# Kernel optimization log

Hardware: AMD Instinct MI355X
Metric: run time of the kernel (lower is better)

## Reference

```python
import jax, jax.numpy as jnp
import numpy as np

N_KERNELS = 5
MUL_FACTOR = 2.0


def setup_inputs() -> dict:
    key = jax.random.key(0)
    k1, k2 = jax.random.split(key)
    x = jax.random.normal(k1, (8192, 64), dtype=jnp.float32)
    y = jax.random.normal(k2, (8192, 64), dtype=jnp.float32)
    return {"x": x, "y": y}


def reference(x, y):
    # bandwidth multipliers: mul_factor ** (arange(n) - n//2) -> [0.25,0.5,1,2,4]
    mults = MUL_FACTOR ** (jnp.arange(N_KERNELS, dtype=jnp.float32) - N_KERNELS // 2)

    z = jnp.concatenate([x, y], axis=0)  # [N, d], N = n + m
    n = x.shape[0]
    N = z.shape[0]

    # squared pairwise L2 distances: ||a||^2 + ||b||^2 - 2 a.b, clamped at 0
    sq = jnp.sum(z * z, axis=-1)  # [N]
    d2 = jnp.maximum(sq[:, None] + sq[None, :] - 2.0 * (z @ z.T), 0.0)  # [N, N]

    # data-dependent bandwidth: sum(d2) / (N^2 - N)
    bw = jnp.sum(d2) / (N * N - N)

    # multi-bandwidth RBF kernel, summed over kernels: [N, N]
    K = jnp.sum(jnp.exp(-d2[None, :, :] / (bw * mults)[:, None, None]), axis=0)

    XX = jnp.mean(K[:n, :n])
    XY = jnp.mean(K[:n, n:])
    YY = jnp.mean(K[n:, n:])
    return XX - 2.0 * XY + YY
```

## Files before the change

kernel.cpp:

```cpp
#include <hip/hip_runtime.h>
#include <hip/hip_bf16.h>

#define D 64

typedef __attribute__((ext_vector_type(8))) _Float16 half8;
typedef __attribute__((ext_vector_type(4))) float floatx4;
typedef __attribute__((ext_vector_type(2))) float f32x2;

typedef __attribute__((address_space(1))) unsigned int gu32_t;
typedef __attribute__((address_space(3))) unsigned int lu32_t;

__global__ __launch_bounds__(256) void k_pre(const float* __restrict__ x, const float* __restrict__ y,
                                             int nx, _Float16* __restrict__ zh,
                                             float* __restrict__ sq, double* __restrict__ Tpart,
                                             float* __restrict__ Spart) {
    int tid = threadIdx.x;
    int lane = tid & 63, wid = tid >> 6;
    int t = blockIdx.x * 256 + tid;
    size_t e = (size_t)t * 8;
    int row = (int)(e >> 6);
    const float* src = (row < nx) ? (x + e) : (y + (e - (size_t)nx * D));
    float4 v0 = ((const float4*)src)[0];
    float4 v1 = ((const float4*)src)[1];
    half8 h;
    h[0]=(_Float16)v0.x; h[1]=(_Float16)v0.y; h[2]=(_Float16)v0.z; h[3]=(_Float16)v0.w;
    h[4]=(_Float16)v1.x; h[5]=(_Float16)v1.y; h[6]=(_Float16)v1.z; h[7]=(_Float16)v1.w;
    *(half8*)(zh + e) = h;
    float p = v0.x*v0.x + v0.y*v0.y + v0.z*v0.z + v0.w*v0.w
            + v1.x*v1.x + v1.y*v1.y + v1.z*v1.z + v1.w*v1.w;
    float s = p;
    s += __shfl_xor(s, 1);
    s += __shfl_xor(s, 2);
    s += __shfl_xor(s, 4);
    if ((tid & 7) == 0) sq[row] = s;

    __shared__ float colbuf[32][64];
    int rib = tid >> 3, cg = tid & 7;
    *(float4*)&colbuf[rib][cg * 8]     = v0;
    *(float4*)&colbuf[rib][cg * 8 + 4] = v1;

    double dp = (double)p;
    dp += __shfl_xor(dp, 1);
    dp += __shfl_xor(dp, 2);
    dp += __shfl_xor(dp, 4);
    dp += __shfl_xor(dp, 8);
    dp += __shfl_xor(dp, 16);
    dp += __shfl_xor(dp, 32);
    __shared__ double redw[4];
    if (lane == 0) redw[wid] = dp;
    __syncthreads();
    if (tid == 0) Tpart[blockIdx.x] = (redw[0] + redw[1]) + (redw[2] + redw[3]);

    if (tid < 64) {
        float cs = 0.f;
#pragma unroll
        for (int r2 = 0; r2 < 32; ++r2) cs += colbuf[r2][tid];
        Spart[blockIdx.x * 64 + tid] = cs;
    }
}

__global__ __launch_bounds__(256) void k_bw(const double* __restrict__ Tpart, int ntp,
                                            const float* __restrict__ Spart, int nsp,
                                            int N, float* __restrict__ cq_p) {
    int t = threadIdx.x;
    double Tp = 0.0;
    for (int b = t; b < ntp; b += 256) Tp += Tpart[b];

    int q = t >> 6, col = t & 63;
    int bpq = nsp >> 2;
    const float* sp = Spart + (size_t)(q * bpq) * 64 + col;
    float c0 = 0.f, c1 = 0.f, c2 = 0.f, c3 = 0.f;
    for (int b = 0; b < bpq; b += 4) {
        c0 += sp[(b + 0) * 64];
        c1 += sp[(b + 1) * 64];
        c2 += sp[(b + 2) * 64];
        c3 += sp[(b + 3) * 64];
    }
    __shared__ float cred[256];
    cred[t] = (c0 + c1) + (c2 + c3);

    __shared__ double red[256];
    red[t] = Tp;
    __syncthreads();
    for (int off = 128; off > 0; off >>= 1) {
        if (t < off) red[t] += red[t + off];
        __syncthreads();
    }
    double T = red[0];
    __shared__ double red2[64];
    if (t < 64) {
        float Sk = cred[t] + cred[t + 64] + cred[t + 128] + cred[t + 192];
        red2[t] = (double)Sk * (double)Sk;
    }
    __syncthreads();
    if (t == 0) {
        double S2 = 0.0;
        for (int i = 0; i < 64; ++i) S2 += red2[i];
        double sumd2 = 2.0 * (double)N * T - 2.0 * S2;
        double bw = sumd2 / ((double)N * (double)N - (double)N);
        cq_p[0] = (float)(1.4426950408889634 / (4.0 * bw));
    }
}

__global__ __launch_bounds__(256, 6) void k_mmd(const _Float16* __restrict__ zh,
                                                const float* __restrict__ sq,
                                                const float* __restrict__ cq_p,
                                                int nb, double* __restrict__ partial) {
    int bid = (nb - 1) - (int)blockIdx.x;
    int g = (int)((sqrtf(1.0f + 2.0f * (float)bid) - 1.0f) * 0.5f);
    while (2 * (g + 1) * (g + 2) <= bid) ++g;
    while (2 * g * (g + 1) > bid) --g;
    int r = bid - 2 * g * (g + 1);
    int gp1 = g + 1;
    int rig = r / gp1;
    int jc  = r - rig * gp1;
    int ib  = 4 * g + rig;

    int jstart = jc * 512;
    int jend   = (ib + 1) * 128;
    if (jend > jstart + 512) jend = jstart + 512;
    int nt = (jend - jstart) >> 6;
    int diag_j = ib * 128;

    int tid  = threadIdx.x;
    int lane = tid & 63;
    int wid  = tid >> 6;
    int i0 = ib * 128 + wid * 32;

    float cq  = cq_p[0];
    f32x2 c2q2 = {2.0f * cq, 2.0f * cq};

    int lrow = lane & 15;
    int c2   = lane >> 4;
    int kb   = c2 * 8;

    const _Float16* ar0 = zh + (size_t)(i0 + lrow) * D + kb;
    half8 a00 = *(const half8*)(ar0);
    half8 a01 = *(const half8*)(ar0 + 32);
    half8 a10 = *(const half8*)(ar0 + 16 * D);
    half8 a11 = *(const half8*)(ar0 + 16 * D + 32);

    int irh = c2 * 4;
    f32x2 na[4];
    na[0] = (f32x2){-sq[i0 + irh + 0] * cq, -sq[i0 + irh + 1] * cq};
    na[1] = (f32x2){-sq[i0 + irh + 2] * cq, -sq[i0 + irh + 3] * cq};
    na[2] = (f32x2){-sq[i0 + 16 + irh + 0] * cq, -sq[i0 + 16 + irh + 1] * cq};
    na[3] = (f32x2){-sq[i0 + 16 + irh + 2] * cq, -sq[i0 + 16 + irh + 3] * cq};

    __shared__ __align__(16) _Float16 bsm[2][64 * 64];
    int srow = tid >> 3;
    int scc  = tid & 7;
    int sc   = scc ^ (srow & 7);
    const char* zbase = (const char*)zh + (size_t)jstart * 128 + srow * 128 + sc * 16;
    char* ldsw = (char*)&bsm[0][0] + wid * 1024;

    auto STAGE = [&](int buf, int tile) {
        const char* src = zbase + (size_t)tile * (64 * 128);
        char* dst = ldsw + buf * 8192;
        __builtin_amdgcn_global_load_lds((const gu32_t*)(const void*)src,
                                         (lu32_t*)(void*)dst, 16, 0, 0);
        __builtin_amdgcn_global_load_lds((const gu32_t*)(const void*)(src + 32 * 128),
                                         (lu32_t*)(void*)(dst + 4096), 16, 0, 0);
    };

    float acc = 0.f;

    STAGE(0, 0);
    __syncthreads();

    for (int t = 0; t < nt; ++t) {
        if (t + 1 < nt) STAGE((t + 1) & 1, t + 1);
        const char* bb = (const char*)&bsm[t & 1][0];
        int j0t = jstart + t * 64;
#pragma unroll
        for (int s = 0; s < 4; ++s) {
            int jr = s * 16 + lrow;
            int swz = jr & 7;
            half8 b0 = *(const half8*)(bb + jr * 128 + ((c2 ^ swz) * 16));
            half8 b1 = *(const half8*)(bb + jr * 128 + (((c2 + 4) ^ swz) * 16));
            float sqj = sq[j0t + s * 16 + lrow];

            floatx4 d0 = {0.f, 0.f, 0.f, 0.f};
            floatx4 d1 = {0.f, 0.f, 0.f, 0.f};
            d0 = __builtin_amdgcn_mfma_f32_16x16x32_f16(a00, b0, d0, 0, 0, 0);
            d0 = __builtin_amdgcn_mfma_f32_16x16x32_f16(a01, b1, d0, 0, 0, 0);
            d1 = __builtin_amdgcn_mfma_f32_16x16x32_f16(a10, b0, d1, 0, 0, 0);
            d1 = __builtin_amdgcn_mfma_f32_16x16x32_f16(a11, b1, d1, 0, 0, 0);

            float nbj = -sqj * cq;
            f32x2 nb2 = {nbj, nbj};

            f32x2 dd[4];
            dd[0] = (f32x2){d0[0], d0[1]};
            dd[1] = (f32x2){d0[2], d0[3]};
            dd[2] = (f32x2){d1[0], d1[1]};
            dd[3] = (f32x2){d1[2], d1[3]};

            f32x2 part2 = {0.f, 0.f};
#pragma unroll
            for (int pk = 0; pk < 4; ++pk) {
                f32x2 u = dd[pk] * c2q2 + (na[pk] + nb2);
                u.x = fminf(u.x, 0.f);
                u.y = fminf(u.y, 0.f);
                f32x2 q;
                q.x = __builtin_amdgcn_exp2f(u.x);
                q.y = __builtin_amdgcn_exp2f(u.y);
                f32x2 m1 = q * q;
                f32x2 m2 = m1 * m1;
                f32x2 m3 = m2 * m2;
                part2 += ((q + m1) + (m2 + m3)) + m3 * m3;
            }
            float wf = ((j0t + s * 16) >= diag_j) ? 1.0f : 2.0f;
            acc = fmaf(part2.x + part2.y, wf, acc);
        }
        __syncthreads();
    }

    double wacc = (double)acc;
    wacc += __shfl_xor(wacc, 1);
    wacc += __shfl_xor(wacc, 2);
    wacc += __shfl_xor(wacc, 4);
    wacc += __shfl_xor(wacc, 8);
    wacc += __shfl_xor(wacc, 16);
    wacc += __shfl_xor(wacc, 32);
    __shared__ double redr[4];
    if (lane == 0) redr[wid] = wacc;
    __syncthreads();
    if (tid == 0) partial[bid] = (redr[0] + redr[1]) + (redr[2] + redr[3]);
}

__global__ __launch_bounds__(256) void k_final(const double* __restrict__ partial, int nb,
                                               int nxTile, int nxChunk,
                                               int nx, int ny, float* __restrict__ out) {
    int t = threadIdx.x;
    double sXX = 0.0, sXY = 0.0, sYY = 0.0;
    for (int p = t; p < nb; p += 256) {
        int g = (int)((sqrtf(1.0f + 2.0f * (float)p) - 1.0f) * 0.5f);
        while (2 * (g + 1) * (g + 2) <= p) ++g;
        while (2 * g * (g + 1) > p) --g;
        int r = p - 2 * g * (g + 1);
        int gp1 = g + 1;
        int rig = r / gp1;
        int jc  = r - rig * gp1;
        int ib  = 4 * g + rig;
        double v = partial[p];
        bool iX = ib < nxTile;
        bool jX = jc < nxChunk;
        if (iX && jX) sXX += v;
        else if (iX != jX) sXY += v;
        else sYY += v;
    }
    __shared__ double r0[256], r1[256], r2[256];
    r0[t] = sXX; r1[t] = sXY; r2[t] = sYY;
    __syncthreads();
    for (int off = 128; off > 0; off >>= 1) {
        if (t < off) {
            r0[t] += r0[t + off];
            r1[t] += r1[t + off];
            r2[t] += r2[t + off];
        }
        __syncthreads();
    }
    if (t == 0) {
        double XX = r0[0] / ((double)nx * (double)nx);
        double XY = r1[0] / (2.0 * (double)nx * (double)ny);
        double YY = r2[0] / ((double)ny * (double)ny);
        out[0] = (float)(XX - 2.0 * XY + YY);
    }
}

extern "C" void kernel_launch(void* const* d_in, const int* in_sizes, int n_in,
                              void* d_out, int out_size, void* d_ws, size_t ws_size,
                              hipStream_t stream) {
    const float* x = (const float*)d_in[0];
    const float* y = (const float*)d_in[1];
    float* out = (float*)d_out;

    int nx = in_sizes[0] / D;
    int ny = in_sizes[1] / D;
    int N  = nx + ny;

    int pre_blocks = (N * D / 8) / 256;
    int nT = N / 128;
    int ngr = nT / 4;
    int nb = 2 * ngr * (ngr + 1);
    int nxTile = nx / 128;
    int nxChunk = nx / 512;

    char* w = (char*)d_ws;
    double* Tpart   = (double*)(w + 0);
    double* partial = (double*)(w + 4096);
    float*  Spart   = (float*) (w + 20992);
    float*  sq      = (float*) (w + 152064);
    float*  cq      = (float*) (w + 217600);
    _Float16* zh    = (_Float16*)(w + 217664);

    k_pre   <<<pre_blocks, 256, 0, stream>>>(x, y, nx, zh, sq, Tpart, Spart);
    k_bw    <<<1, 256, 0, stream>>>(Tpart, pre_blocks, Spart, pre_blocks, N, cq);
    k_mmd   <<<nb, 256, 0, stream>>>(zh, sq, cq, nb, partial);
    k_final <<<1, 256, 0, stream>>>(partial, nb, nxTile, nxChunk, nx, ny, out);
}
```

Before: 127.2 us.

## Triple-buffer smaller B tiles, stage sq in LDS, and replace partial reductions with atomics

The main kernel now stages 32-row B tiles into a three-deep LDS ring, waiting on vmcnt with a raw s_barrier instead of a full __syncthreads each step. It also preloads the column squared norms into LDS and raises occupancy launch bounds from 6 to 8. Per-block partials for the bandwidth statistics and the final XX/XY/YY sums become double atomics plus a memset, which simplifies the reduction kernels. The X/Y split is now hardcoded (ib<64, jc<16), so it only matches nx=8192, and the extra memset adds a launch.

New measurement: 131.3 us. 3.2% more time.

```diff
diff --git a/kernel.cpp b/kernel.cpp
--- a/kernel.cpp
+++ b/kernel.cpp
@@ -12,8 +12,8 @@
 
 __global__ __launch_bounds__(256) void k_pre(const float* __restrict__ x, const float* __restrict__ y,
                                              int nx, _Float16* __restrict__ zh,
-                                             float* __restrict__ sq, double* __restrict__ Tpart,
-                                             float* __restrict__ Spart) {
+                                             float* __restrict__ sq, double* __restrict__ Tsum,
+                                             double* __restrict__ colsum) {
     int tid = threadIdx.x;
     int lane = tid & 63, wid = tid >> 6;
     int t = blockIdx.x * 256 + tid;
@@ -49,63 +49,40 @@
     __shared__ double redw[4];
     if (lane == 0) redw[wid] = dp;
     __syncthreads();
-    if (tid == 0) Tpart[blockIdx.x] = (redw[0] + redw[1]) + (redw[2] + redw[3]);
+    if (tid == 0) atomicAdd(Tsum, (redw[0] + redw[1]) + (redw[2] + redw[3]));
 
     if (tid < 64) {
         float cs = 0.f;
 #pragma unroll
         for (int r2 = 0; r2 < 32; ++r2) cs += colbuf[r2][tid];
-        Spart[blockIdx.x * 64 + tid] = cs;
-    }
-}
-
-__global__ __launch_bounds__(256) void k_bw(const double* __restrict__ Tpart, int ntp,
-                                            const float* __restrict__ Spart, int nsp,
-                                            int N, float* __restrict__ cq_p) {
+        atomicAdd(&colsum[tid], (double)cs);
+    }
+}
+
+__global__ __launch_bounds__(64) void k_bw(const double* __restrict__ Tsum,
+                                           const double* __restrict__ colsum,
+                                           int N, float* __restrict__ cq_p) {
     int t = threadIdx.x;
-    double Tp = 0.0;
-    for (int b = t; b < ntp; b += 256) Tp += Tpart[b];
-
-    int q = t >> 6, col = t & 63;
-    int bpq = nsp >> 2;
-    const float* sp = Spart + (size_t)(q * bpq) * 64 + col;
-    float c0 = 0.f, c1 = 0.f, c2 = 0.f, c3 = 0.f;
-    for (int b = 0; b < bpq; b += 4) {
-        c0 += sp[(b + 0) * 64];
-        c1 += sp[(b + 1) * 64];
-        c2 += sp[(b + 2) * 64];
-        c3 += sp[(b + 3) * 64];
-    }
-    __shared__ float cred[256];
-    cred[t] = (c0 + c1) + (c2 + c3);
-
-    __shared__ double red[256];
-    red[t] = Tp;
-    __syncthreads();
-    for (int off = 128; off > 0; off >>= 1) {
-        if (t < off) red[t] += red[t + off];
-        __syncthreads();
-    }
-    double T = red[0];
-    __shared__ double red2[64];
-    if (t < 64) {
-        float Sk = cred[t] + cred[t + 64] + cred[t + 128] + cred[t + 192];
-        red2[t] = (double)Sk * (double)Sk;
-    }
-    __syncthreads();
+    double Sk = colsum[t];
+    double v = Sk * Sk;
+    v += __shfl_xor(v, 1);
+    v += __shfl_xor(v, 2);
+    v += __shfl_xor(v, 4);
+    v += __shfl_xor(v, 8);
+    v += __shfl_xor(v, 16);
+    v += __shfl_xor(v, 32);
     if (t == 0) {
-        double S2 = 0.0;
-        for (int i = 0; i < 64; ++i) S2 += red2[i];
-        double sumd2 = 2.0 * (double)N * T - 2.0 * S2;
+        double T = Tsum[0];
+        double sumd2 = 2.0 * (double)N * T - 2.0 * v;
         double bw = sumd2 / ((double)N * (double)N - (double)N);
         cq_p[0] = (float)(1.4426950408889634 / (4.0 * bw));
     }
 }
 
-__global__ __launch_bounds__(256, 6) void k_mmd(const _Float16* __restrict__ zh,
+__global__ __launch_bounds__(256, 8) void k_mmd(const _Float16* __restrict__ zh,
                                                 const float* __restrict__ sq,
                                                 const float* __restrict__ cq_p,
-                                                int nb, double* __restrict__ partial) {
+                                                int nb, double* __restrict__ accs) {
     int bid = (nb - 1) - (int)blockIdx.x;
     int g = (int)((sqrtf(1.0f + 2.0f * (float)bid) - 1.0f) * 0.5f);
     while (2 * (g + 1) * (g + 2) <= bid) ++g;
@@ -119,7 +96,7 @@
     int jstart = jc * 512;
     int jend   = (ib + 1) * 128;
     if (jend > jstart + 512) jend = jstart + 512;
-    int nt = (jend - jstart) >> 6;
+    int nt = (jend - jstart) >> 5;
     int diag_j = ib * 128;
 
     int tid  = threadIdx.x;
@@ -132,9 +109,8 @@
 
     int lrow = lane & 15;
     int c2   = lane >> 4;
-    int kb   = c2 * 8;
-
-    const _Float16* ar0 = zh + (size_t)(i0 + lrow) * D + kb;
+
+    const _Float16* ar0 = zh + (size_t)(i0 + lrow) * D + c2 * 8;
     half8 a00 = *(const half8*)(ar0);
     half8 a01 = *(const half8*)(ar0 + 32);
     half8 a10 = *(const half8*)(ar0 + 16 * D);
@@ -147,38 +123,45 @@
     na[2] = (f32x2){-sq[i0 + 16 + irh + 0] * cq, -sq[i0 + 16 + irh + 1] * cq};
     na[3] = (f32x2){-sq[i0 + 16 + irh + 2] * cq, -sq[i0 + 16 + irh + 3] * cq};
 
-    __shared__ __align__(16) _Float16 bsm[2][64 * 64];
+    __shared__ __align__(16) _Float16 bsm[3][32 * 64];
+    __shared__ float sql[512];
+    __shared__ double redr[4];
+
+    int width = nt << 5;
+    for (int k = tid; k < width; k += 256) sql[k] = sq[jstart + k];
+
     int srow = tid >> 3;
-    int scc  = tid & 7;
-    int sc   = scc ^ (srow & 7);
-    const char* zbase = (const char*)zh + (size_t)jstart * 128 + srow * 128 + sc * 16;
+    int slot = tid & 7;
+    int sc   = slot ^ (srow & 7);
+    const char* zlane = (const char*)zh + (size_t)jstart * 128 + srow * 128 + sc * 16;
     char* ldsw = (char*)&bsm[0][0] + wid * 1024;
 
-    auto STAGE = [&](int buf, int tile) {
-        const char* src = zbase + (size_t)tile * (64 * 128);
-        char* dst = ldsw + buf * 8192;
-        __builtin_amdgcn_global_load_lds((const gu32_t*)(const void*)src,
-                                         (lu32_t*)(void*)dst, 16, 0, 0);
-        __builtin_amdgcn_global_load_lds((const gu32_t*)(const void*)(src + 32 * 128),
-                                         (lu32_t*)(void*)(dst + 4096), 16, 0, 0);
+    auto STAGE = [&](int buf, int t) {
+        __builtin_amdgcn_global_load_lds((const gu32_t*)(const void*)(zlane + (size_t)t * 4096),
+                                         (lu32_t*)(void*)(ldsw + buf * 4096), 16, 0, 0);
     };
 
     float acc = 0.f;
 
     STAGE(0, 0);
+    STAGE(1, 1);
     __syncthreads();
 
+    int cur = 0;
     for (int t = 0; t < nt; ++t) {
-        if (t + 1 < nt) STAGE((t + 1) & 1, t + 1);
-        const char* bb = (const char*)&bsm[t & 1][0];
-        int j0t = jstart + t * 64;
+        if (t + 2 < nt) {
+            int sbuf = (cur == 0) ? 2 : cur - 1;
+            STAGE(sbuf, t + 2);
+        }
+        const char* bb = (const char*)&bsm[cur][0];
+        int j0t = jstart + t * 32;
 #pragma unroll
-        for (int s = 0; s < 4; ++s) {
+        for (int s = 0; s < 2; ++s) {
             int jr = s * 16 + lrow;
             int swz = jr & 7;
             half8 b0 = *(const half8*)(bb + jr * 128 + ((c2 ^ swz) * 16));
             half8 b1 = *(const half8*)(bb + jr * 128 + (((c2 + 4) ^ swz) * 16));
-            float sqj = sq[j0t + s * 16 + lrow];
+            float sqj = sql[t * 32 + s * 16 + lrow];
 
             floatx4 d0 = {0.f, 0.f, 0.f, 0.f};
             floatx4 d1 = {0.f, 0.f, 0.f, 0.f};
@@ -189,7 +172,6 @@
 
             float nbj = -sqj * cq;
             f32x2 nb2 = {nbj, nbj};
-
             f32x2 dd[4];
             dd[0] = (f32x2){d0[0], d0[1]};
             dd[1] = (f32x2){d0[2], d0[3]};
@@ -213,7 +195,17 @@
             float wf = ((j0t + s * 16) >= diag_j) ? 1.0f : 2.0f;
             acc = fmaf(part2.x + part2.y, wf, acc);
         }
-        __syncthreads();
+
+        if (t + 1 < nt) {
+            if (t + 2 < nt) {
+                asm volatile("s_waitcnt vmcnt(1)" ::: "memory");
+            } else {
+                asm volatile("s_waitcnt vmcnt(0)" ::: "memory");
+            }
+            __builtin_amdgcn_sched_barrier(0);
+            __builtin_amdgcn_s_barrier();
+        }
+        cur = (cur == 2) ? 0 : cur + 1;
     }
 
     double wacc = (double)acc;
@@ -223,48 +215,23 @@
     wacc += __shfl_xor(wacc, 8);
     wacc += __shfl_xor(wacc, 16);
     wacc += __shfl_xor(wacc, 32);
-    __shared__ double redr[4];
     if (lane == 0) redr[wid] = wacc;
     __syncthreads();
-    if (tid == 0) partial[bid] = (redr[0] + redr[1]) + (redr[2] + redr[3]);
-}
-
-__global__ __launch_bounds__(256) void k_final(const double* __restrict__ partial, int nb,
-                                               int nxTile, int nxChunk,
-                                               int nx, int ny, float* __restrict__ out) {
-    int t = threadIdx.x;
-    double sXX = 0.0, sXY = 0.0, sYY = 0.0;
-    for (int p = t; p < nb; p += 256) {
-        int g = (int)((sqrtf(1.0f + 2.0f * (float)p) - 1.0f) * 0.5f);
-        while (2 * (g + 1) * (g + 2) <= p) ++g;
-        while (2 * g * (g + 1) > p) --g;
-        int r = p - 2 * g * (g + 1);
-        int gp1 = g + 1;
-        int rig = r / gp1;
-        int jc  = r - rig * gp1;
-        int ib  = 4 * g + rig;
-        double v = partial[p];
-        bool iX = ib < nxTile;
-        bool jX = jc < nxChunk;
-        if (iX && jX) sXX += v;
-        else if (iX != jX) sXY += v;
-        else sYY += v;
-    }
-    __shared__ double r0[256], r1[256], r2[256];
-    r0[t] = sXX; r1[t] = sXY; r2[t] = sYY;
-    __syncthreads();
-    for (int off = 128; off > 0; off >>= 1) {
-        if (t < off) {
-            r0[t] += r0[t + off];
-            r1[t] += r1[t + off];
-            r2[t] += r2[t + off];
-        }
-        __syncthreads();
-    }
-    if (t == 0) {
-        double XX = r0[0] / ((double)nx * (double)nx);
-        double XY = r1[0] / (2.0 * (double)nx * (double)ny);
-        double YY = r2[0] / ((double)ny * (double)ny);
+    if (tid == 0) {
+        double tot = (redr[0] + redr[1]) + (redr[2] + redr[3]);
+        bool iX = ib < 64;
+        bool jX = jc < 16;
+        double* tgt = (iX && jX) ? &accs[0] : ((iX != jX) ? &accs[1] : &accs[2]);
+        atomicAdd(tgt, tot);
+    }
+}
+
+__global__ __launch_bounds__(64) void k_fin(const double* __restrict__ accs,
+                                            int nx, int ny, float* __restrict__ out) {
+    if (threadIdx.x == 0) {
+        double XX = accs[0] / ((double)nx * (double)nx);
+        double XY = accs[1] / (2.0 * (double)nx * (double)ny);
+        double YY = accs[2] / ((double)ny * (double)ny);
         out[0] = (float)(XX - 2.0 * XY + YY);
     }
 }
@@ -284,19 +251,18 @@
     int nT = N / 128;
     int ngr = nT / 4;
     int nb = 2 * ngr * (ngr + 1);
-    int nxTile = nx / 128;
-    int nxChunk = nx / 512;
 
     char* w = (char*)d_ws;
-    double* Tpart   = (double*)(w + 0);
-    double* partial = (double*)(w + 4096);
-    float*  Spart   = (float*) (w + 20992);
-    float*  sq      = (float*) (w + 152064);
-    float*  cq      = (float*) (w + 217600);
-    _Float16* zh    = (_Float16*)(w + 217664);
-
-    k_pre   <<<pre_blocks, 256, 0, stream>>>(x, y, nx, zh, sq, Tpart, Spart);
-    k_bw    <<<1, 256, 0, stream>>>(Tpart, pre_blocks, Spart, pre_blocks, N, cq);
-    k_mmd   <<<nb, 256, 0, stream>>>(zh, sq, cq, nb, partial);
-    k_final <<<1, 256, 0, stream>>>(partial, nb, nxTile, nxChunk, nx, ny, out);
-}
+    double* accs   = (double*)(w + 0);
+    double* Tsum   = (double*)(w + 24);
+    double* colsum = (double*)(w + 32);
+    float*  cq     = (float*) (w + 544);
+    float*  sq     = (float*) (w + 608);
+    _Float16* zh   = (_Float16*)(w + 66144);
+
+    hipMemsetAsync(w, 0, 544, stream);
+    k_pre <<<pre_blocks, 256, 0, stream>>>(x, y, nx, zh, sq, Tsum, colsum);
+    k_bw  <<<1, 64, 0, stream>>>(Tsum, colsum, N, cq);
+    k_mmd <<<nb, 256, 0, stream>>>(zh, sq, cq, nb, accs);
+    k_fin <<<1, 64, 0, stream>>>(accs, nx, ny, out);
+}
```
